# Kernel tuning notes

Measured on AMD Instinct MI355X. Metric: run time of the kernel, lower is better.

The kernel has to match this reference:

```python
import jax, jax.numpy as jnp
import numpy as np

Q_STEPS, Q_TOKENS = 16, 64
KV_STEPS, KV_TOKENS = 64, 64
WINDOW = 2
TOPK = 32
DIM = 512
BATCH = 8
NUM_CONTEXTS = 2


def build_local_mask(q_steps, q_tokens, kv_steps, kv_tokens, window):
    # centers: nearest kv step for each query step
    centers = np.round(np.linspace(0, kv_steps - 1, q_steps)).astype(np.int64)
    steps = np.arange(kv_steps)
    allowed = np.abs(steps[None, :] - centers[:, None]) <= window  # [q_steps, kv_steps]
    allowed = np.repeat(np.repeat(allowed, q_tokens, axis=0), kv_tokens, axis=1)
    return jnp.where(jnp.asarray(allowed), 0.0, -jnp.inf).astype(jnp.float32)


MASK = build_local_mask(Q_STEPS, Q_TOKENS, KV_STEPS, KV_TOKENS, WINDOW)


def setup_inputs() -> dict:
    key = jax.random.key(0)
    ks = jax.random.split(key, 12)
    s = 1.0 / np.sqrt(DIM)
    return {
        "query": jax.random.normal(ks[0], (BATCH, Q_STEPS, Q_TOKENS, DIM), jnp.float32),
        "source": jax.random.normal(ks[1], (BATCH, KV_STEPS, KV_TOKENS, DIM), jnp.float32),
        "ctx1": jax.random.normal(ks[2], (BATCH, DIM), jnp.float32),
        "ctx2": jax.random.normal(ks[3], (BATCH, DIM), jnp.float32),
        "Wq": jax.random.normal(ks[4], (DIM, DIM), jnp.float32) * s,
        "bq": jnp.zeros((DIM,), jnp.float32),
        "Wk": jax.random.normal(ks[5], (DIM, DIM), jnp.float32) * s,
        "bk": jnp.zeros((DIM,), jnp.float32),
        "Wv": jax.random.normal(ks[6], (DIM, DIM), jnp.float32) * s,
        "bv": jnp.zeros((DIM,), jnp.float32),
        "Wo": jax.random.normal(ks[7], (DIM, DIM), jnp.float32) * s,
        "bo": jnp.zeros((DIM,), jnp.float32),
        "Wc": jax.random.normal(ks[8], (NUM_CONTEXTS * DIM, 2 * DIM), jnp.float32) * s,
        "bc": jnp.zeros((2 * DIM,), jnp.float32),
    }


def reference(query, source, ctx1, ctx2, Wq, bq, Wk, bk, Wv, bv, Wo, bo, Wc, bc):
    B = query.shape[0]
    # CrossScaleCondition: fuse contexts -> per-batch FiLM params gamma, beta [B, dim]
    fused = jnp.concatenate([ctx1, ctx2], axis=-1)          # [B, num_contexts*dim]
    gb = fused @ Wc + bc                                     # [B, 2*dim]
    gamma, beta = jnp.split(gb, 2, axis=-1)

    q_flat = query.reshape(B, Q_STEPS * Q_TOKENS, DIM)       # [B, Lq, d]
    src_flat = source.reshape(B, KV_STEPS * KV_TOKENS, DIM)  # [B, Lkv, d]

    q_mod = q_flat * (1.0 + gamma[:, None, :]) + beta[:, None, :]
    q = q_mod @ Wq + bq
    k = src_flat @ Wk + bk
    v = src_flat @ Wv + bv

    scores = jnp.einsum('bqd,bkd->bqk', q, k) / jnp.sqrt(jnp.float32(DIM))
    scores = scores + MASK[None]                             # local window mask

    topk_scores, topk_idx = jax.lax.top_k(scores, TOPK)      # [B, Lq, k]
    selected_v = jax.vmap(lambda vb, ib: vb[ib])(v, topk_idx)  # [B, Lq, k, d]

    attn = jax.nn.softmax(topk_scores, axis=-1)
    out = jnp.einsum('bqk,bqkd->bqd', attn, selected_v)
    out = out @ Wo + bo
    return out.reshape(B, Q_STEPS, Q_TOKENS, DIM)
```

## Files before the change

### kernel.cpp

```cpp
#include <hip/hip_runtime.h>

#define NWIN 320
#define SCORE_SCALE 0.04419417382415922f

__constant__ int CENTERS[16] = {0,4,8,13,17,21,25,29,34,38,42,46,50,55,59,63};

typedef __attribute__((ext_vector_type(8))) short v8s;
typedef __attribute__((ext_vector_type(4))) float v4f;

__device__ __forceinline__ float bflo(unsigned u) { return __uint_as_float(u << 16); }
__device__ __forceinline__ float bfhi(unsigned u) { return __uint_as_float(u & 0xffff0000u); }
__device__ __forceinline__ float bf2f(unsigned short h) { return __uint_as_float(((unsigned)h) << 16); }
__device__ __forceinline__ unsigned short f2bf(float x) {
  unsigned u = __float_as_uint(x);
  unsigned r = 0x7fffu + ((u >> 16) & 1u);
  return (unsigned short)((u + r) >> 16);
}

__device__ __forceinline__ int t64_off(int r, int k) {
  return ((r & 31) << 7) + (((((r >> 5) << 2) | (k >> 3)) ^ (r & 7)) << 4) + ((k & 7) << 1);
}
__device__ __forceinline__ int frag_off(int r, int g) {
  return ((r & 31) << 7) + (((((r >> 5) << 2) | g) ^ (r & 7)) << 4);
}

__device__ __forceinline__ void gload_lds16(const void* g, void* l) {
  __builtin_amdgcn_global_load_lds((const __attribute__((address_space(1))) unsigned int*)g,
                                   (__attribute__((address_space(3))) unsigned int*)l, 16, 0, 0);
}

__device__ __forceinline__ void cvt8pair(float4 a, float4 b, uint4& hi4, uint4& lo4) {
  float v[8] = {a.x, a.y, a.z, a.w, b.x, b.y, b.z, b.w};
  unsigned short h[8], l[8];
  #pragma unroll
  for (int e = 0; e < 8; ++e) {
    h[e] = f2bf(v[e]);
    l[e] = f2bf(v[e] - bf2f(h[e]));
  }
  hi4.x = (unsigned)h[0] | ((unsigned)h[1] << 16);
  hi4.y = (unsigned)h[2] | ((unsigned)h[3] << 16);
  hi4.z = (unsigned)h[4] | ((unsigned)h[5] << 16);
  hi4.w = (unsigned)h[6] | ((unsigned)h[7] << 16);
  lo4.x = (unsigned)l[0] | ((unsigned)l[1] << 16);
  lo4.y = (unsigned)l[2] | ((unsigned)l[3] << 16);
  lo4.z = (unsigned)l[4] | ((unsigned)l[5] << 16);
  lo4.w = (unsigned)l[6] | ((unsigned)l[7] << 16);
}

__device__ __forceinline__ uint4 cvt8hi(float4 a, float4 b) {
  uint4 r;
  r.x = (unsigned)f2bf(a.x) | ((unsigned)f2bf(a.y) << 16);
  r.y = (unsigned)f2bf(a.z) | ((unsigned)f2bf(a.w) << 16);
  r.z = (unsigned)f2bf(b.x) | ((unsigned)f2bf(b.y) << 16);
  r.w = (unsigned)f2bf(b.z) | ((unsigned)f2bf(b.w) << 16);
  return r;
}

__device__ __forceinline__ uint2 cvt4(float4 a) {
  uint2 r;
  r.x = (unsigned)f2bf(a.x) | ((unsigned)f2bf(a.y) << 16);
  r.y = (unsigned)f2bf(a.z) | ((unsigned)f2bf(a.w) << 16);
  return r;
}

__global__ __launch_bounds__(256) void prep1_kernel(
    const float* __restrict__ ctx1, const float* __restrict__ ctx2,
    const float* __restrict__ Wc,  float* __restrict__ part,
    const float* __restrict__ Wk,  const float* __restrict__ bq, float* __restrict__ u,
    const float* __restrict__ Wq,
    unsigned short* __restrict__ Wqh, unsigned short* __restrict__ Wql,
    unsigned short* __restrict__ Wkh, unsigned short* __restrict__ Wkl,
    const float* __restrict__ Wv, const float* __restrict__ Wo,
    unsigned short* __restrict__ Wvt, unsigned short* __restrict__ Wot)
{
  __shared__ char img[32768];
  const int bid = blockIdx.x;
  const int tid = threadIdx.x;

  if (bid < 256) {
    const int b = bid >> 5, sl = (bid >> 2) & 7, jq = bid & 3;
    const int j = jq * 256 + tid;
    const int i0 = sl * 128;
    float acc = 0.f;
    #pragma unroll 4
    for (int t = 0; t < 128; ++t) {
      const int i = i0 + t;
      const float f = (i < 512) ? ctx1[b * 512 + i] : ctx2[b * 512 + i - 512];
      acc = fmaf(f, Wc[(size_t)i * 1024 + j], acc);
    }
    part[(b * 8 + sl) * 1024 + j] = acc;
  } else if (bid < 384) {
    const int d = (bid - 256) * 4 + (tid >> 6);
    const int lane = tid & 63;
    float4 a0 = *(const float4*)&Wk[(size_t)d * 512 + lane * 8];
    float4 a1 = *(const float4*)&Wk[(size_t)d * 512 + lane * 8 + 4];
    float4 c0 = *(const float4*)&bq[lane * 8];
    float4 c1 = *(const float4*)&bq[lane * 8 + 4];
    float s = a0.x*c0.x + a0.y*c0.y + a0.z*c0.z + a0.w*c0.w
            + a1.x*c1.x + a1.y*c1.y + a1.z*c1.z + a1.w*c1.w;
    #pragma unroll
    for (int off = 32; off > 0; off >>= 1) s += __shfl_xor(s, off, 64);
    if (lane == 0) u[d] = s * SCORE_SCALE;
  } else if (bid < 640) {
    const int b = bid - 384;
    const int mat = b >> 7;
    const float* Wsrc = mat ? Wk : Wq;
    unsigned short* Wh = mat ? Wkh : Wqh;
    unsigned short* Wl = mat ? Wkl : Wql;
    const size_t e0 = (((size_t)(b & 127) * 256) + tid) * 8;
    float4 x0 = *(const float4*)&Wsrc[e0];
    float4 x1 = *(const float4*)&Wsrc[e0 + 4];
    uint4 h4, l4;
    cvt8pair(x0, x1, h4, l4);
    *(uint4*)&Wh[e0] = h4;
    *(uint4*)&Wl[e0] = l4;
  } else {
    const int cb = bid - 640;
    const int ktile = cb & 15;
    const int mat   = cb >> 4;
    const float* W = mat ? Wo : Wv;
    unsigned short* Dt = mat ? Wot : Wvt;
    const int k  = tid >> 3;
    const int nt = tid & 7;
    #pragma unroll
    for (int e4 = 0; e4 < 16; ++e4) {
      float4 w = *(const float4*)&W[(size_t)(ktile * 32 + k) * 512 + nt * 64 + e4 * 4];
      float vv[4] = {w.x, w.y, w.z, w.w};
      #pragma unroll
      for (int c = 0; c < 4; ++c) {
        const int n = e4 * 4 + c;
        *(unsigned short*)(img + nt * 4096 + t64_off(n, k)) = f2bf(vv[c]);
      }
    }
    __syncthreads();
    const uint4* src = (const uint4*)img;
    uint4* dst = (uint4*)((char*)Dt + (size_t)ktile * 32768);
    for (int i = tid; i < 2048; i += 256) dst[i] = src[i];
  }
}

__global__ __launch_bounds__(256) void prep2_kernel(
    const unsigned short* __restrict__ Wqh, const unsigned short* __restrict__ Wql,
    const unsigned short* __restrict__ Wkh, const unsigned short* __restrict__ Wkl,
    unsigned short* __restrict__ Gt,
    const float* __restrict__ part, const float* __restrict__ bc,
    float* __restrict__ gb)
{
  const int bid = blockIdx.x;
  const int tid = threadIdx.x;

  if (bid < 256) {
    const int lane = tid & 63, l15 = lane & 15, g = lane >> 4;
    const int wave = tid >> 6;
    const int t  = (bid << 2) | wave;
    const int ti = t >> 5, tj = t & 31;
    const int ib = ti << 4, jb = tj << 4;
    const size_t arow = (size_t)(ib + l15) * 512 + (g << 3);
    const size_t brow = (size_t)(jb + l15) * 512 + (g << 3);

    v4f acc = (v4f){0.f, 0.f, 0.f, 0.f};
    #pragma unroll 4
    for (int kk = 0; kk < 16; ++kk) {
      const int kd = kk * 32;
      const v8s ah = *(const v8s*)&Wqh[arow + kd];
      const v8s al = *(const v8s*)&Wql[arow + kd];
      const v8s bh = *(const v8s*)&Wkh[brow + kd];
      const v8s bl = *(const v8s*)&Wkl[brow + kd];
      acc = __builtin_amdgcn_mfma_f32_16x16x32_bf16(ah, bh, acc, 0, 0, 0);
      acc = __builtin_amdgcn_mfma_f32_16x16x32_bf16(al, bh, acc, 0, 0, 0);
      acc = __builtin_amdgcn_mfma_f32_16x16x32_bf16(ah, bl, acc, 0, 0, 0);
    }
    #pragma unroll
    for (int k = 0; k < 4; ++k) {
      const int gi = ib + (g << 2) + k;
      const int gj = jb + l15;
      const float v = acc[k] * SCORE_SCALE;
      const unsigned short hi = f2bf(v);
      const unsigned short lo = f2bf(v - bf2f(hi));
      const int toff = t64_off(gj & 63, gi & 31);
      *(unsigned short*)((char*)Gt + ((size_t)((gi >> 5) * 8 + (gj >> 6)) << 12) + toff) = hi;
      *(unsigned short*)((char*)Gt + ((size_t)(((gi >> 5) + 16) * 8 + (gj >> 6)) << 12) + toff) = lo;
    }
  } else {
    const int rb = bid - 256;
    const int b = rb >> 2, jq = rb & 3;
    const int j = jq * 256 + tid;
    float acc = bc[j];
    #pragma unroll
    for (int sl = 0; sl < 8; ++sl) acc += part[(b * 8 + sl) * 1024 + j];
    gb[b * 1024 + j] = acc;
  }
}

__global__ __launch_bounds__(256) void proj_split(
    const float* __restrict__ A, const unsigned short* __restrict__ Bt,
    const float* __restrict__ bias, const float* __restrict__ gb,
    unsigned short* __restrict__ Qgt)
{
  __shared__ char smem[49152];
  char* const LAh = smem;
  char* const LAl = smem + 8192;
  char* const LBh = smem + 16384;
  char* const LBl = smem + 32768;

  const int tid  = threadIdx.x;
  const int lane = tid & 63, l15 = lane & 15, g = lane >> 4;
  const int wave = tid >> 6, wm = wave >> 1, wn = wave & 1;
  const int bid = blockIdx.x;
  const int xcd = bid & 7, idx = bid >> 3;
  const int mBlk = (idx & 15) | (xcd << 4);
  const int nBlk = idx >> 4;

  const int sr = tid >> 2;
  const int sq = tid & 3;
  const size_t arow = (size_t)(mBlk * 64 + sr) * 512 + sq * 8;
  const int gbbase = ((mBlk >> 4) * 1024) + sq * 8;
  const int awoff = t64_off(sr, sq * 8);

  int aoff[2], boff[4];
  #pragma unroll
  for (int fm = 0; fm < 2; ++fm) aoff[fm] = frag_off(wm * 32 + fm * 16 + l15, g);
  #pragma unroll
  for (int fn = 0; fn < 4; ++fn) {
    const int n = wn * 64 + fn * 16 + l15;
    boff[fn] = ((n >> 6) << 12) + frag_off(n & 63, g);
  }

  v4f acc[2][4];
  #pragma unroll
  for (int fm = 0; fm < 2; ++fm)
    #pragma unroll
    for (int fn = 0; fn < 4; ++fn) acc[fm][fn] = (v4f){0.f, 0.f, 0.f, 0.f};

  for (int tk = 0; tk < 8; ++tk) {
    const int kd = tk * 64;
    #pragma unroll
    for (int ks = 0; ks < 2; ++ks) {
      const int tk32 = tk * 2 + ks;
      const char* gsh = (const char*)Bt + ((size_t)(tk32 * 8 + nBlk * 2) << 12) + (size_t)tid * 16;
      const char* gsl = (const char*)Bt + ((size_t)((tk32 + 16) * 8 + nBlk * 2) << 12) + (size_t)tid * 16;
      #pragma unroll
      for (int i = 0; i < 2; ++i) {
        gload_lds16(gsh + i * 4096, LBh + ks * 8192 + (wave << 10) + i * 4096);
        gload_lds16(gsl + i * 4096, LBl + ks * 8192 + (wave << 10) + i * 4096);
      }
    }
    #pragma unroll
    for (int ks = 0; ks < 2; ++ks) {
      const int kds = kd + ks * 32;
      float4 x0 = *(const float4*)&A[arow + kds];
      float4 x1 = *(const float4*)&A[arow + kds + 4];
      float4 g0 = *(const float4*)&gb[gbbase + kds];
      float4 g1 = *(const float4*)&gb[gbbase + kds + 4];
      float4 b0 = *(const float4*)&gb[gbbase + 512 + kds];
      float4 b1 = *(const float4*)&gb[gbbase + 512 + kds + 4];
      x0.x = fmaf(x0.x, 1.f + g0.x, b0.x); x0.y = fmaf(x0.y, 1.f + g0.y, b0.y);
      x0.z = fmaf(x0.z, 1.f + g0.z, b0.z); x0.w = fmaf(x0.w, 1.f + g0.w, b0.w);
      x1.x = fmaf(x1.x, 1.f + g1.x, b1.x); x1.y = fmaf(x1.y, 1.f + g1.y, b1.y);
      x1.z = fmaf(x1.z, 1.f + g1.z, b1.z); x1.w = fmaf(x1.w, 1.f + g1.w, b1.w);
      uint4 hi4, lo4;
      cvt8pair(x0, x1, hi4, lo4);
      *(uint4*)(LAh + ks * 4096 + awoff) = hi4;
      *(uint4*)(LAl + ks * 4096 + awoff) = lo4;
    }
    __syncthreads();
    #pragma unroll
    for (int ks = 0; ks < 2; ++ks) {
      const v8s ah0 = *(const v8s*)(LAh + ks * 4096 + aoff[0]);
      const v8s ah1 = *(const v8s*)(LAh + ks * 4096 + aoff[1]);
      const v8s al0 = *(const v8s*)(LAl + ks * 4096 + aoff[0]);
      const v8s al1 = *(const v8s*)(LAl + ks * 4096 + aoff[1]);
      #pragma unroll
      for (int fn = 0; fn < 4; ++fn) {
        const v8s bh = *(const v8s*)(LBh + ks * 8192 + boff[fn]);
        const v8s bl = *(const v8s*)(LBl + ks * 8192 + boff[fn]);
        acc[0][fn] = __builtin_amdgcn_mfma_f32_16x16x32_bf16(ah0, bh, acc[0][fn], 0, 0, 0);
        acc[1][fn] = __builtin_amdgcn_mfma_f32_16x16x32_bf16(ah1, bh, acc[1][fn], 0, 0, 0);
        acc[0][fn] = __builtin_amdgcn_mfma_f32_16x16x32_bf16(al0, bh, acc[0][fn], 0, 0, 0);
        acc[1][fn] = __builtin_amdgcn_mfma_f32_16x16x32_bf16(al1, bh, acc[1][fn], 0, 0, 0);
        acc[0][fn] = __builtin_amdgcn_mfma_f32_16x16x32_bf16(ah0, bl, acc[0][fn], 0, 0, 0);
        acc[1][fn] = __builtin_amdgcn_mfma_f32_16x16x32_bf16(ah1, bl, acc[1][fn], 0, 0, 0);
      }
    }
    __syncthreads();
  }

  #pragma unroll
  for (int fn = 0; fn < 4; ++fn) {
    const int col = nBlk * 128 + wn * 64 + fn * 16 + l15;
    const float bv = bias[col];
    const int kt = col >> 5;
    const int kk = col & 31;
    #pragma unroll
    for (int fm = 0; fm < 2; ++fm) {
      const int r0 = wm * 32 + fm * 16 + g * 4;
      #pragma unroll
      for (int k = 0; k < 4; ++k) {
        const float vv = acc[fm][fn][k] + bv;
        const unsigned short hi = f2bf(vv);
        const unsigned short lo = f2bf(vv - bf2f(hi));
        const int toff = t64_off(r0 + k, kk);
        *(unsigned short*)((char*)Qgt + ((size_t)(kt * 128 + mBlk) << 12) + toff) = hi;
        *(unsigned short*)((char*)Qgt + ((size_t)((kt + 16) * 128 + mBlk) << 12) + toff) = lo;
      }
    }
  }
}

__global__ __launch_bounds__(512) void proj_v(
    const float* __restrict__ A, const unsigned short* __restrict__ Bt,
    const float* __restrict__ bias, unsigned short* __restrict__ Cb)
{
  __shared__ char smem[8192 + 65536];
  char* const LA = smem;
  char* const LB = smem + 8192;

  const int tid  = threadIdx.x;
  const int lane = tid & 63, l15 = lane & 15, g = lane >> 4;
  const int wave = tid >> 6, wm = wave >> 2, wn = wave & 3;
  const int mBlk = blockIdx.x;

  const int sr  = tid >> 3;
  const int sq4 = tid & 7;
  const size_t arow = (size_t)(mBlk * 64 + sr) * 512 + sq4 * 4;
  const int awoff = t64_off(sr, sq4 * 4);

  int aoff[2], boff[8];
  #pragma unroll
  for (int fm = 0; fm < 2; ++fm) aoff[fm] = frag_off(wm * 32 + fm * 16 + l15, g);
  #pragma unroll
  for (int fn = 0; fn < 8; ++fn) {
    const int n = wn * 128 + fn * 16 + l15;
    boff[fn] = ((n >> 6) << 12) + frag_off(n & 63, g);
  }

  v4f acc[2][8];
  #pragma unroll
  for (int fm = 0; fm < 2; ++fm)
    #pragma unroll
    for (int fn = 0; fn < 8; ++fn) acc[fm][fn] = (v4f){0.f, 0.f, 0.f, 0.f};

  for (int tk = 0; tk < 8; ++tk) {
    const int kd = tk * 64;
    #pragma unroll
    for (int ks = 0; ks < 2; ++ks) {
      const char* gs = (const char*)Bt + ((size_t)(tk * 2 + ks) << 15) + (wave << 12) + (lane << 4);
      char* ld = LB + (ks << 15) + (wave << 12);
      #pragma unroll
      for (int i = 0; i < 4; ++i) gload_lds16(gs + (i << 10), ld + (i << 10));
    }
    #pragma unroll
    for (int ks = 0; ks < 2; ++ks) {
      float4 x = *(const float4*)&A[arow + kd + ks * 32];
      *(uint2*)(LA + (ks << 12) + awoff) = cvt4(x);
    }
    __syncthreads();
    #pragma unroll
    for (int ks = 0; ks < 2; ++ks) {
      const v8s a0 = *(const v8s*)(LA + (ks << 12) + aoff[0]);
      const v8s a1 = *(const v8s*)(LA + (ks << 12) + aoff[1]);
      #pragma unroll
      for (int fn = 0; fn < 8; ++fn) {
        const v8s bb = *(const v8s*)(LB + (ks << 15) + boff[fn]);
        acc[0][fn] = __builtin_amdgcn_mfma_f32_16x16x32_bf16(a0, bb, acc[0][fn], 0, 0, 0);
        acc[1][fn] = __builtin_amdgcn_mfma_f32_16x16x32_bf16(a1, bb, acc[1][fn], 0, 0, 0);
      }
    }
    __syncthreads();
  }

  #pragma unroll
  for (int fn = 0; fn < 8; ++fn) {
    const int col = wn * 128 + fn * 16 + l15;
    const float bv = bias[col];
    #pragma unroll
    for (int fm = 0; fm < 2; ++fm) {
      const int r0 = mBlk * 64 + wm * 32 + fm * 16 + g * 4;
      #pragma unroll
      for (int k = 0; k < 4; ++k)
        Cb[(size_t)(r0 + k) * 512 + col] = f2bf(acc[fm][fn][k] + bv);
    }
  }
}

__global__ __launch_bounds__(256) void proj_o(
    const float* __restrict__ A, const unsigned short* __restrict__ Bt,
    const float* __restrict__ bias, float* __restrict__ Cf)
{
  __shared__ char smem[12288];
  char* const LA = smem;
  char* const LB = smem + 4096;

  const int tid  = threadIdx.x;
  const int lane = tid & 63, l15 = lane & 15, g = lane >> 4;
  const int wave = tid >> 6, wm = wave >> 1, wn = wave & 1;
  const int bid = blockIdx.x;
  const int xcd = bid & 7, idx = bid >> 3;
  const int mBlk = (idx & 15) | (xcd << 4);
  const int nBlk = idx >> 4;

  const int sr = tid >> 2;
  const int sq = tid & 3;
  const size_t arow = (size_t)(mBlk * 64 + sr) * 512 + sq * 8;
  const int awoff = t64_off(sr, sq * 8);

  int aoff[2], boff[4];
  #pragma unroll
  for (int fm = 0; fm < 2; ++fm) aoff[fm] = frag_off(wm * 32 + fm * 16 + l15, g);
  #pragma unroll
  for (int fn = 0; fn < 4; ++fn) {
    const int n = wn * 64 + fn * 16 + l15;
    boff[fn] = ((n >> 6) << 12) + frag_off(n & 63, g);
  }

  v4f acc[2][4];
  #pragma unroll
  for (int fm = 0; fm < 2; ++fm)
    #pragma unroll
    for (int fn = 0; fn < 4; ++fn) acc[fm][fn] = (v4f){0.f, 0.f, 0.f, 0.f};

  for (int tk = 0; tk < 16; ++tk) {
    const int kd = tk * 32;
    {
      const char* gs = (const char*)Bt + ((size_t)tk << 15) + ((size_t)nBlk << 13) + (size_t)tid * 16;
      #pragma unroll
      for (int i = 0; i < 2; ++i)
        gload_lds16(gs + i * 4096, LB + (wave << 10) + i * 4096);
    }
    {
      float4 x0 = *(const float4*)&A[arow + kd];
      float4 x1 = *(const float4*)&A[arow + kd + 4];
      *(uint4*)(LA + awoff) = cvt8hi(x0, x1);
    }
    __syncthreads();
    const v8s a0 = *(const v8s*)(LA + aoff[0]);
    const v8s a1 = *(const v8s*)(LA + aoff[1]);
    #pragma unroll
    for (int fn = 0; fn < 4; ++fn) {
      const v8s bb = *(const v8s*)(LB + boff[fn]);
      acc[0][fn] = __builtin_amdgcn_mfma_f32_16x16x32_bf16(a0, bb, acc[0][fn], 0, 0, 0);
      acc[1][fn] = __builtin_amdgcn_mfma_f32_16x16x32_bf16(a1, bb, acc[1][fn], 0, 0, 0);
    }
    __syncthreads();
  }

  #pragma unroll
  for (int fn = 0; fn < 4; ++fn) {
    const int col = nBlk * 128 + wn * 64 + fn * 16 + l15;
    const float bv = bias[col];
    #pragma unroll
    for (int fm = 0; fm < 2; ++fm) {
      const int r0 = mBlk * 64 + wm * 32 + fm * 16 + g * 4;
      #pragma unroll
      for (int k = 0; k < 4; ++k)
        Cf[(size_t)(r0 + k) * 512 + col] = acc[fm][fn][k] + bv;
    }
  }
}

__global__ __launch_bounds__(256) void scores_mfma(
    const unsigned short* __restrict__ Qgt, const float* __restrict__ SRC,
    float* __restrict__ S)
{
  const int bs = blockIdx.y;
  const int s = bs & 15, b = bs >> 4;
  const int c  = CENTERS[s];
  const int lo = (c - 2 > 0) ? c - 2 : 0;
  const int hi = (c + 2 < 63) ? c + 2 : 63;
  if ((int)blockIdx.x > hi - lo) return;

  __shared__ char smem[16384];
  char* const LAh = smem;
  char* const LAl = smem + 4096;
  char* const LBh = smem + 8192;
  char* const LBl = smem + 12288;

  const int tid = threadIdx.x;
  const int lane = tid & 63, l15 = lane & 15, g = lane >> 4;
  const int wave = tid >> 6, wm = wave >> 1, wn = wave & 1;
  const int kvrow0 = (b << 12) + ((lo + (int)blockIdx.x) << 6);
  const int qbase  = bs << 6;
  const int sr = tid >> 2, sq = tid & 3;
  const size_t krow = (size_t)(kvrow0 + sr) * 512 + sq * 8;
  const int awoff = t64_off(sr, sq * 8);

  int aoff[2], boff[2];
  #pragma unroll
  for (int f = 0; f < 2; ++f) {
    aoff[f] = frag_off(wm * 32 + f * 16 + l15, g);
    boff[f] = frag_off(wn * 32 + f * 16 + l15, g);
  }

  v4f acc[2][2];
  #pragma unroll
  for (int i = 0; i < 2; ++i)
    #pragma unroll
    for (int j = 0; j < 2; ++j) acc[i][j] = (v4f){0.f, 0.f, 0.f, 0.f};

  for (int tk = 0; tk < 16; ++tk) {
    const int kd = tk * 32;
    {
      const char* gah = (const char*)Qgt + ((size_t)(tk * 128 + bs) << 12) + (size_t)tid * 16;
      const char* gal = (const char*)Qgt + ((size_t)((tk + 16) * 128 + bs) << 12) + (size_t)tid * 16;
      gload_lds16(gah, LAh + (wave << 10));
      gload_lds16(gal, LAl + (wave << 10));
    }
    {
      float4 y0 = *(const float4*)&SRC[krow + kd];
      float4 y1 = *(const float4*)&SRC[krow + kd + 4];
      uint4 bhi, blo;
      cvt8pair(y0, y1, bhi, blo);
      *(uint4*)(LBh + awoff) = bhi;
      *(uint4*)(LBl + awoff) = blo;
    }
    __syncthreads();
    const v8s a0h = *(const v8s*)(LAh + aoff[0]);
    const v8s a1h = *(const v8s*)(LAh + aoff[1]);
    const v8s a0l = *(const v8s*)(LAl + aoff[0]);
    const v8s a1l = *(const v8s*)(LAl + aoff[1]);
    const v8s b0h = *(const v8s*)(LBh + boff[0]);
    const v8s b1h = *(const v8s*)(LBh + boff[1]);
    const v8s b0l = *(const v8s*)(LBl + boff[0]);
    const v8s b1l = *(const v8s*)(LBl + boff[1]);
    acc[0][0] = __builtin_amdgcn_mfma_f32_16x16x32_bf16(a0h, b0h, acc[0][0], 0, 0, 0);
    acc[0][1] = __builtin_amdgcn_mfma_f32_16x16x32_bf16(a0h, b1h, acc[0][1], 0, 0, 0);
    acc[1][0] = __builtin_amdgcn_mfma_f32_16x16x32_bf16(a1h, b0h, acc[1][0], 0, 0, 0);
    acc[1][1] = __builtin_amdgcn_mfma_f32_16x16x32_bf16(a1h, b1h, acc[1][1], 0, 0, 0);
    acc[0][0] = __builtin_amdgcn_mfma_f32_16x16x32_bf16(a0l, b0h, acc[0][0], 0, 0, 0);
    acc[0][1] = __builtin_amdgcn_mfma_f32_16x16x32_bf16(a0l, b1h, acc[0][1], 0, 0, 0);
    acc[1][0] = __builtin_amdgcn_mfma_f32_16x16x32_bf16(a1l, b0h, acc[1][0], 0, 0, 0);
    acc[1][1] = __builtin_amdgcn_mfma_f32_16x16x32_bf16(a1l, b1h, acc[1][1], 0, 0, 0);
    acc[0][0] = __builtin_amdgcn_mfma_f32_16x16x32_bf16(a0h, b0l, acc[0][0], 0, 0, 0);
    acc[0][1] = __builtin_amdgcn_mfma_f32_16x16x32_bf16(a0h, b1l, acc[0][1], 0, 0, 0);
    acc[1][0] = __builtin_amdgcn_mfma_f32_16x16x32_bf16(a1h, b0l, acc[1][0], 0, 0, 0);
    acc[1][1] = __builtin_amdgcn_mfma_f32_16x16x32_bf16(a1h, b1l, acc[1][1], 0, 0, 0);
    __syncthreads();
  }

  #pragma unroll
  for (int fn = 0; fn < 2; ++fn) {
    const int cl = wn * 32 + fn * 16 + l15;
    const int colS = ((int)blockIdx.x << 6) + cl;
    #pragma unroll
    for (int fm = 0; fm < 2; ++fm) {
      const int r0 = qbase + wm * 32 + fm * 16 + g * 4;
      #pragma unroll
      for (int k = 0; k < 4; ++k)
        S[(size_t)(r0 + k) * NWIN + colS] = acc[fm][fn][k];
    }
  }
}

__global__ __launch_bounds__(256) void topk_pv(
    const float* __restrict__ S, const unsigned short* __restrict__ Vb,
    float* __restrict__ O)
{
  __shared__ int   sel_i[4][32];
  __shared__ float sel_p[4][32];

  const int lane = threadIdx.x & 63;
  const int wv   = threadIdx.x >> 6;
  const int b0   = blockIdx.x;
  const int grp  = (b0 & 7) + ((b0 >> 7) << 3);
  const int blk  = (b0 >> 3) & 15;
  const int row  = (((grp << 4) + blk) << 2) + wv;
  const int b    = row >> 10;
  const int s    = (row >> 6) & 15;
  const int c    = CENTERS[s];
  const int lo   = (c - 2 > 0) ? c - 2 : 0;
  const int hi   = (c + 2 < 63) ? c + 2 : 63;
  const int L    = (hi - lo + 1) << 6;
  const size_t vbase = ((size_t)b << 12) + ((size_t)lo << 6);

  const float* srow = S + (size_t)row * NWIN;
  float f[5]; unsigned uo[5];
  #pragma unroll
  for (int j = 0; j < 5; ++j) {
    const int idx = lane + (j << 6);
    const float v = (idx < L) ? srow[idx] : -__builtin_inff();
    f[j] = v;
    const unsigned fb = __float_as_uint(v);
    uo[j] = (fb & 0x80000000u) ? ~fb : (fb | 0x80000000u);
  }

  float m = f[0];
  #pragma unroll
  for (int j = 1; j < 5; ++j) m = fmaxf(m, f[j]);
  #pragma unroll
  for (int off = 32; off > 0; off >>= 1) m = fmaxf(m, __shfl_xor(m, off, 64));

  unsigned T = 0u;
  for (int bit = 31; bit >= 0; --bit) {
    const unsigned cand = T | (1u << bit);
    int cnt = 0;
    #pragma unroll
    for (int j = 0; j < 5; ++j)
      cnt += __popcll(__ballot(uo[j] >= cand));
    if (cnt >= 32) T = cand;
  }

  int base = 0;
  #pragma unroll
  for (int j = 0; j < 5; ++j) {
    const unsigned long long gm = __ballot(uo[j] > T);
    if (uo[j] > T) {
      const int rank = base + __builtin_amdgcn_mbcnt_hi(
          (unsigned)(gm >> 32), __builtin_amdgcn_mbcnt_lo((unsigned)gm, 0));
      sel_i[wv][rank] = lane + (j << 6);
      sel_p[wv][rank] = __expf(f[j] - m);
    }
    base += __popcll(gm);
  }
  #pragma unroll
  for (int j = 0; j < 5; ++j) {
    const unsigned long long em = __ballot(uo[j] == T);
    if (uo[j] == T) {
      const int er = base + __builtin_amdgcn_mbcnt_hi(
          (unsigned)(em >> 32), __builtin_amdgcn_mbcnt_lo((unsigned)em, 0));
      if (er < 32) {
        sel_i[wv][er] = lane + (j << 6);
        sel_p[wv][er] = __expf(f[j] - m);
      }
    }
    base += __popcll(em);
  }

  asm volatile("s_waitcnt lgkmcnt(0)" ::: "memory");

  const int   si = sel_i[wv][lane & 31];
  const float sp = sel_p[wv][lane & 31];
  float dp = (lane < 32) ? sp : 0.f;
  #pragma unroll
  for (int off = 32; off > 0; off >>= 1) dp += __shfl_xor(dp, off, 64);

  float oacc[8] = {0.f,0.f,0.f,0.f,0.f,0.f,0.f,0.f};
  #pragma unroll
  for (int t = 0; t < 32; ++t) {
    const int   idx_t = __builtin_amdgcn_readlane(si, t);
    const float p_t   = __uint_as_float(
        (unsigned)__builtin_amdgcn_readlane((int)__float_as_uint(sp), t));
    const unsigned short* vrow = Vb + ((vbase + (size_t)idx_t) << 9);
    #pragma unroll
    for (int e = 0; e < 4; ++e) {
      const unsigned raw = *(const unsigned*)&vrow[(lane << 1) + (e << 7)];
      oacc[2*e]     = fmaf(p_t, bflo(raw), oacc[2*e]);
      oacc[2*e + 1] = fmaf(p_t, bfhi(raw), oacc[2*e + 1]);
    }
  }

  const float inv = 1.0f / dp;
  float* orow = O + ((size_t)row << 9);
  #pragma unroll
  for (int e = 0; e < 4; ++e) {
    float2 o2 = make_float2(oacc[2*e] * inv, oacc[2*e + 1] * inv);
    *(float2*)&orow[(lane << 1) + (e << 7)] = o2;
  }
}

extern "C" void kernel_launch(void* const* d_in, const int* in_sizes, int n_in,
                              void* d_out, int out_size, void* d_ws, size_t ws_size,
                              hipStream_t stream)
{
  (void)in_sizes; (void)n_in; (void)out_size; (void)ws_size;

  const float* query  = (const float*)d_in[0];
  const float* source = (const float*)d_in[1];
  const float* ctx1   = (const float*)d_in[2];
  const float* ctx2   = (const float*)d_in[3];
  const float* Wq     = (const float*)d_in[4];
  const float* bq     = (const float*)d_in[5];
  const float* Wk     = (const float*)d_in[6];
  const float* Wv     = (const float*)d_in[8];
  const float* bv     = (const float*)d_in[9];
  const float* Wo     = (const float*)d_in[10];
  const float* bo     = (const float*)d_in[11];
  const float* Wc     = (const float*)d_in[12];
  const float* bc     = (const float*)d_in[13];
  float* out = (float*)d_out;

  char* ws = (char*)d_ws;
  unsigned short* Qgt  = (unsigned short*)(ws);
  unsigned short* v    = (unsigned short*)(ws + 16777216);
  float*          S    = (float*)(ws + 50331648);
  float*          ctx  = (float*)(ws + 60817408);
  unsigned short* Gt   = (unsigned short*)(ws + 77594624);
  unsigned short* Wvt  = (unsigned short*)(ws + 78643200);
  unsigned short* Wot  = (unsigned short*)(ws + 79167488);
  float*          gb   = (float*)(ws + 79691776);
  float*          part = (float*)(ws + 79724544);
  float*          u    = (float*)(ws + 79986688);
  unsigned short* Wqh  = (unsigned short*)(ws + 79988736);
  unsigned short* Wql  = (unsigned short*)(ws + 80513024);
  unsigned short* Wkh  = (unsigned short*)(ws + 81037312);
  unsigned short* Wkl  = (unsigned short*)(ws + 81561600);

  prep1_kernel<<<672, 256, 0, stream>>>(ctx1, ctx2, Wc, part, Wk, bq, u, Wq,
                                        Wqh, Wql, Wkh, Wkl, Wv, Wo, Wvt, Wot);
  prep2_kernel<<<288, 256, 0, stream>>>(Wqh, Wql, Wkh, Wkl, Gt, part, bc, gb);
  proj_split<<<512, 256, 0, stream>>>(query, Gt, u, gb, Qgt);
  proj_v<<<512, 512, 0, stream>>>(source, Wvt, bv, v);
  scores_mfma<<<dim3(5, 128), 256, 0, stream>>>(Qgt, source, S);
  topk_pv<<<2048, 256, 0, stream>>>(S, v, ctx);
  proj_o<<<512, 256, 0, stream>>>(ctx, Wot, bo, out);
}
```

Before: 145.9 us.

## Apply V projection after top-k gather instead of projecting full source

```diff
diff --git a/kernel.cpp b/kernel.cpp
--- a/kernel.cpp
+++ b/kernel.cpp
@@ -53,13 +53,6 @@
   r.y = (unsigned)f2bf(a.z) | ((unsigned)f2bf(a.w) << 16);
   r.z = (unsigned)f2bf(b.x) | ((unsigned)f2bf(b.y) << 16);
   r.w = (unsigned)f2bf(b.z) | ((unsigned)f2bf(b.w) << 16);
-  return r;
-}
-
-__device__ __forceinline__ uint2 cvt4(float4 a) {
-  uint2 r;
-  r.x = (unsigned)f2bf(a.x) | ((unsigned)f2bf(a.y) << 16);
-  r.y = (unsigned)f2bf(a.z) | ((unsigned)f2bf(a.w) << 16);
   return r;
 }
 
@@ -307,82 +300,6 @@
   }
 }
 
-__global__ __launch_bounds__(512) void proj_v(
-    const float* __restrict__ A, const unsigned short* __restrict__ Bt,
-    const float* __restrict__ bias, unsigned short* __restrict__ Cb)
-{
-  __shared__ char smem[8192 + 65536];
-  char* const LA = smem;
-  char* const LB = smem + 8192;
-
-  const int tid  = threadIdx.x;
-  const int lane = tid & 63, l15 = lane & 15, g = lane >> 4;
-  const int wave = tid >> 6, wm = wave >> 2, wn = wave & 3;
-  const int mBlk = blockIdx.x;
-
-  const int sr  = tid >> 3;
-  const int sq4 = tid & 7;
-  const size_t arow = (size_t)(mBlk * 64 + sr) * 512 + sq4 * 4;
-  const int awoff = t64_off(sr, sq4 * 4);
-
-  int aoff[2], boff[8];
-  #pragma unroll
-  for (int fm = 0; fm < 2; ++fm) aoff[fm] = frag_off(wm * 32 + fm * 16 + l15, g);
-  #pragma unroll
-  for (int fn = 0; fn < 8; ++fn) {
-    const int n = wn * 128 + fn * 16 + l15;
-    boff[fn] = ((n >> 6) << 12) + frag_off(n & 63, g);
-  }
-
-  v4f acc[2][8];
-  #pragma unroll
-  for (int fm = 0; fm < 2; ++fm)
-    #pragma unroll
-    for (int fn = 0; fn < 8; ++fn) acc[fm][fn] = (v4f){0.f, 0.f, 0.f, 0.f};
-
-  for (int tk = 0; tk < 8; ++tk) {
-    const int kd = tk * 64;
-    #pragma unroll
-    for (int ks = 0; ks < 2; ++ks) {
-      const char* gs = (const char*)Bt + ((size_t)(tk * 2 + ks) << 15) + (wave << 12) + (lane << 4);
-      char* ld = LB + (ks << 15) + (wave << 12);
-      #pragma unroll
-      for (int i = 0; i < 4; ++i) gload_lds16(gs + (i << 10), ld + (i << 10));
-    }
-    #pragma unroll
-    for (int ks = 0; ks < 2; ++ks) {
-      float4 x = *(const float4*)&A[arow + kd + ks * 32];
-      *(uint2*)(LA + (ks << 12) + awoff) = cvt4(x);
-    }
-    __syncthreads();
-    #pragma unroll
-    for (int ks = 0; ks < 2; ++ks) {
-      const v8s a0 = *(const v8s*)(LA + (ks << 12) + aoff[0]);
-      const v8s a1 = *(const v8s*)(LA + (ks << 12) + aoff[1]);
-      #pragma unroll
-      for (int fn = 0; fn < 8; ++fn) {
-        const v8s bb = *(const v8s*)(LB + (ks << 15) + boff[fn]);
-        acc[0][fn] = __builtin_amdgcn_mfma_f32_16x16x32_bf16(a0, bb, acc[0][fn], 0, 0, 0);
-        acc[1][fn] = __builtin_amdgcn_mfma_f32_16x16x32_bf16(a1, bb, acc[1][fn], 0, 0, 0);
-      }
-    }
-    __syncthreads();
-  }
-
-  #pragma unroll
-  for (int fn = 0; fn < 8; ++fn) {
-    const int col = wn * 128 + fn * 16 + l15;
-    const float bv = bias[col];
-    #pragma unroll
-    for (int fm = 0; fm < 2; ++fm) {
-      const int r0 = mBlk * 64 + wm * 32 + fm * 16 + g * 4;
-      #pragma unroll
-      for (int k = 0; k < 4; ++k)
-        Cb[(size_t)(r0 + k) * 512 + col] = f2bf(acc[fm][fn][k] + bv);
-    }
-  }
-}
-
 __global__ __launch_bounds__(256) void proj_o(
     const float* __restrict__ A, const unsigned short* __restrict__ Bt,
     const float* __restrict__ bias, float* __restrict__ Cf)
@@ -552,7 +469,7 @@
 }
 
 __global__ __launch_bounds__(256) void topk_pv(
-    const float* __restrict__ S, const unsigned short* __restrict__ Vb,
+    const float* __restrict__ S, const float* __restrict__ SRC,
     float* __restrict__ O)
 {
   __shared__ int   sel_i[4][32];
@@ -639,12 +556,12 @@
     const int   idx_t = __builtin_amdgcn_readlane(si, t);
     const float p_t   = __uint_as_float(
         (unsigned)__builtin_amdgcn_readlane((int)__float_as_uint(sp), t));
-    const unsigned short* vrow = Vb + ((vbase + (size_t)idx_t) << 9);
+    const float* vrow = SRC + ((vbase + (size_t)idx_t) << 9);
     #pragma unroll
     for (int e = 0; e < 4; ++e) {
-      const unsigned raw = *(const unsigned*)&vrow[(lane << 1) + (e << 7)];
-      oacc[2*e]     = fmaf(p_t, bflo(raw), oacc[2*e]);
-      oacc[2*e + 1] = fmaf(p_t, bfhi(raw), oacc[2*e + 1]);
+      const float2 v2 = *(const float2*)&vrow[(lane << 1) + (e << 7)];
+      oacc[2*e]     = fmaf(p_t, v2.x, oacc[2*e]);
+      oacc[2*e + 1] = fmaf(p_t, v2.y, oacc[2*e + 1]);
     }
   }
 
@@ -680,7 +597,7 @@
 
   char* ws = (char*)d_ws;
   unsigned short* Qgt  = (unsigned short*)(ws);
-  unsigned short* v    = (unsigned short*)(ws + 16777216);
+  float*          tmp  = (float*)(ws + 16777216);
   float*          S    = (float*)(ws + 50331648);
   float*          ctx  = (float*)(ws + 60817408);
   unsigned short* Gt   = (unsigned short*)(ws + 77594624);
@@ -698,8 +615,8 @@
                                         Wqh, Wql, Wkh, Wkl, Wv, Wo, Wvt, Wot);
   prep2_kernel<<<288, 256, 0, stream>>>(Wqh, Wql, Wkh, Wkl, Gt, part, bc, gb);
   proj_split<<<512, 256, 0, stream>>>(query, Gt, u, gb, Qgt);
-  proj_v<<<512, 512, 0, stream>>>(source, Wvt, bv, v);
   scores_mfma<<<dim3(5, 128), 256, 0, stream>>>(Qgt, source, S);
-  topk_pv<<<2048, 256, 0, stream>>>(S, v, ctx);
-  proj_o<<<512, 256, 0, stream>>>(ctx, Wot, bo, out);
-}
+  topk_pv<<<2048, 256, 0, stream>>>(S, source, ctx);
+  proj_o<<<512, 256, 0, stream>>>(ctx, Wvt, bv, tmp);
+  proj_o<<<512, 256, 0, stream>>>(tmp, Wot, bo, out);
+}
```

Measured after the change: 154.9 us. +6.2%, slower.
